# Kernel tuning notes

Hardware: AMD Instinct MI355X
Metric: run time of the kernel (lower is better)

Reference implementation:

```python
import jax, jax.numpy as jnp
import numpy as np

HEADS = 8
MODEL_DIM = 64
EPS = 1e-5


def _layernorm(x, gamma, beta):
    mu = jnp.mean(x, axis=-1, keepdims=True)
    var = jnp.var(x, axis=-1, keepdims=True)
    return (x - mu) * jax.lax.rsqrt(var + EPS) * gamma + beta


def setup_inputs() -> dict:
    key = jax.random.key(0)
    ks = jax.random.split(key, 5)
    bs, h, w, in_dim = 8, 32, 32, 512
    hd = HEADS * MODEL_DIM  # 512
    s = 0.02
    return {
        "x": jax.random.normal(ks[0], (bs, h, w, in_dim), jnp.float32),
        "Wq": jax.random.normal(ks[1], (in_dim, hd), jnp.float32) * s,
        "Wk": jax.random.normal(ks[2], (in_dim, hd), jnp.float32) * s,
        "Wv": jax.random.normal(ks[3], (in_dim, hd), jnp.float32) * s,
        "Wo": jax.random.normal(ks[4], (hd, in_dim), jnp.float32) * s,
        "gamma": jnp.ones((in_dim,), jnp.float32),
        "beta": jnp.zeros((in_dim,), jnp.float32),
    }


def reference(x, Wq, Wk, Wv, Wo, gamma, beta):
    bs, h, w, in_dim = x.shape
    # pre_norm=True: normalize first; residual uses the normalized x (as in original)
    xn = _layernorm(x, gamma, beta)
    Q = (xn @ Wq).reshape(bs, h, w, HEADS, MODEL_DIM)
    K = (xn @ Wk).reshape(bs, h, w, HEADS, MODEL_DIM)
    V = (xn @ Wv).reshape(bs, h, w, HEADS, MODEL_DIM)
    # full (h,w) x (h,w) correlation per head
    corr = jnp.einsum('bijhd,bklhd->bijhkl', Q, K) / jnp.sqrt(
        jnp.asarray(MODEL_DIM, x.dtype))
    cshape = corr.shape
    attn = jax.nn.softmax(corr.reshape(*cshape[:-2], -1), axis=-1).reshape(cshape)
    logits = jnp.einsum('bijhkl,bklhd->bijhd', attn, V).reshape(bs, h, w, -1)
    out = logits @ Wo + xn
    return out, attn
```

## Files before the change

### kernel.cpp

```cpp
#include <hip/hip_runtime.h>
#include <hip/hip_bf16.h>

typedef __attribute__((ext_vector_type(8))) short bf16x8;
typedef __attribute__((ext_vector_type(4))) short s16x4;
typedef __attribute__((ext_vector_type(4))) float f32x4;

#define DIM 512
#define NH 8
#define HD 64
#define SEQ 1024
#define NB 8
#define ROWS (NB*SEQ)

__device__ __forceinline__ short f2bf(float f) {
  union { float f; unsigned u; } v; v.f = f;
  unsigned r = v.u + 0x7fffu + ((v.u >> 16) & 1u);
  return (short)(r >> 16);
}
__device__ __forceinline__ float bf2f(short s) {
  union { unsigned u; float f; } v; v.u = ((unsigned)(unsigned short)s) << 16;
  return v.f;
}
__device__ __forceinline__ f32x4 mfma16(bf16x8 a, bf16x8 b, f32x4 c) {
  return __builtin_amdgcn_mfma_f32_16x16x32_bf16(a, b, c, 0, 0, 0);
}
__device__ __forceinline__ void gload16(const void* g, void* l) {
  __builtin_amdgcn_global_load_lds(
      (const __attribute__((address_space(1))) unsigned int*)g,
      (__attribute__((address_space(3))) unsigned int*)l, 16, 0, 0);
}
__device__ __forceinline__ void lds_barrier() {
  __builtin_amdgcn_sched_barrier(0);
  asm volatile("s_waitcnt lgkmcnt(0)" ::: "memory");
  __builtin_amdgcn_s_barrier();
  __builtin_amdgcn_sched_barrier(0);
}

__global__ __launch_bounds__(256) void prep_kernel(
    const float* __restrict__ x, const float* __restrict__ gamma,
    const float* __restrict__ beta, short* __restrict__ xnb,
    const float* __restrict__ Wq, const float* __restrict__ Wk,
    const float* __restrict__ Wv, const float* __restrict__ Wo,
    short* __restrict__ WqkvT, short* __restrict__ WoT) {
  __shared__ float tl[64 * 65];
  const int t = threadIdx.x;
  if (blockIdx.x < 2048) {
    const int row = blockIdx.x * 4 + (t >> 6);
    const int lane = t & 63;
    const float4* xr = reinterpret_cast<const float4*>(x + (size_t)row * DIM);
    const float4 a = xr[lane * 2], b2 = xr[lane * 2 + 1];
    float s = a.x + a.y + a.z + a.w + b2.x + b2.y + b2.z + b2.w;
    float sq = a.x*a.x + a.y*a.y + a.z*a.z + a.w*a.w +
               b2.x*b2.x + b2.y*b2.y + b2.z*b2.z + b2.w*b2.w;
    for (int off = 1; off < 64; off <<= 1) {
      s += __shfl_xor(s, off);
      sq += __shfl_xor(sq, off);
    }
    const float mean = s * (1.0f / DIM);
    const float var = sq * (1.0f / DIM) - mean * mean;
    const float rs = rsqrtf(var + 1e-5f);
    const float4 ga = reinterpret_cast<const float4*>(gamma)[lane * 2];
    const float4 gb = reinterpret_cast<const float4*>(gamma)[lane * 2 + 1];
    const float4 ba = reinterpret_cast<const float4*>(beta)[lane * 2];
    const float4 bb = reinterpret_cast<const float4*>(beta)[lane * 2 + 1];
    union { bf16x8 v; short sh[8]; } o;
    o.sh[0] = f2bf((a.x - mean) * rs * ga.x + ba.x);
    o.sh[1] = f2bf((a.y - mean) * rs * ga.y + ba.y);
    o.sh[2] = f2bf((a.z - mean) * rs * ga.z + ba.z);
    o.sh[3] = f2bf((a.w - mean) * rs * ga.w + ba.w);
    o.sh[4] = f2bf((b2.x - mean) * rs * gb.x + bb.x);
    o.sh[5] = f2bf((b2.y - mean) * rs * gb.y + bb.y);
    o.sh[6] = f2bf((b2.z - mean) * rs * gb.z + bb.z);
    o.sh[7] = f2bf((b2.w - mean) * rs * gb.w + bb.w);
    *reinterpret_cast<bf16x8*>(xnb + (size_t)row * DIM + lane * 8) = o.v;
  } else {
    const int bb = blockIdx.x - 2048;
    const int y = bb >> 6;
    const float* W = (y == 0) ? Wq : (y == 1) ? Wk : (y == 2) ? Wv : Wo;
    const int tile = bb & 63;
    const int k0 = (tile >> 3) * 64, n0 = (tile & 7) * 64;
#pragma unroll
    for (int i = 0; i < 16; ++i) {
      const int idx = i * 256 + t;
      const int k = idx >> 6, n = idx & 63;
      tl[n * 65 + k] = W[(size_t)(k0 + k) * 512 + n0 + n];
    }
    __syncthreads();
#pragma unroll
    for (int i = 0; i < 16; ++i) {
      const int idx = i * 256 + t;
      const int n = idx >> 6, k = idx & 63;
      const short v = f2bf(tl[n * 65 + k]);
      if (y < 3) WqkvT[(size_t)(y * 512 + n0 + n) * 512 + k0 + k] = v;
      else       WoT[(size_t)(n0 + n) * 512 + k0 + k] = v;
    }
  }
}

#define GEMM64_MAIN(A_, BT_, m0_, n0_)                                        \
  f32x4 acc[4][4] = {};                                                       \
  {                                                                           \
    const int srow = 8 * w + (lane >> 3);                                     \
    const int sseg = lane & 7;                                                \
    for (int kb = 0; kb < 512; kb += 64) {                                    \
      __syncthreads();                                                        \
      _Pragma("unroll")                                                       \
      for (int p = 0; p < 4; ++p) {                                           \
        const int r = 32 * p + srow;                                          \
        const int gs = 8 * (sseg ^ (r & 7));                                  \
        gload16(A_ + (size_t)(m0_ + r) * 512 + kb + gs,                       \
                &As[(32 * p + 8 * w) * 64]);                                  \
        gload16(BT_ + (size_t)(n0_ + r) * 512 + kb + gs,                      \
                &Bs[(32 * p + 8 * w) * 64]);                                  \
      }                                                                       \
      __syncthreads();                                                        \
      _Pragma("unroll")                                                       \
      for (int half = 0; half < 2; ++half) {                                  \
        bf16x8 af[4], bfr[4];                                                 \
        _Pragma("unroll")                                                     \
        for (int i = 0; i < 4; ++i) {                                         \
          const int ra = 64 * wr + 16 * i + c16;                              \
          af[i] = *reinterpret_cast<const bf16x8*>(                           \
              &As[ra * 64 + 8 * ((4 * half + g) ^ (ra & 7))]);                \
          const int rb = 64 * wc + 16 * i + c16;                              \
          bfr[i] = *reinterpret_cast<const bf16x8*>(                          \
              &Bs[rb * 64 + 8 * ((4 * half + g) ^ (rb & 7))]);                \
        }                                                                     \
        _Pragma("unroll")                                                     \
        for (int i = 0; i < 4; ++i)                                           \
          _Pragma("unroll")                                                   \
          for (int j = 0; j < 4; ++j)                                         \
            acc[i][j] = mfma16(af[i], bfr[j], acc[i][j]);                     \
      }                                                                       \
    }                                                                         \
  }

__global__ __launch_bounds__(256) void gemm_qkv(const short* __restrict__ A,
    const short* __restrict__ BT, short* __restrict__ Qo,
    short* __restrict__ Ko, short* __restrict__ VtF) {
  __shared__ short As[128 * 64];
  __shared__ short Bs[128 * 64];
  const int m0 = blockIdx.x * 128, n0 = blockIdx.y * 128;
  const int t = threadIdx.x, w = t >> 6, lane = t & 63, g = lane >> 4, c16 = lane & 15;
  const int wr = w >> 1, wc = w & 1;
  GEMM64_MAIN(A, BT, m0, n0)
  const int z = n0 >> 9;
  const int nl = n0 & 511;
  if (z < 2) {
    short* O = (z == 0) ? Qo : Ko;
#pragma unroll
    for (int i = 0; i < 4; ++i)
#pragma unroll
      for (int j = 0; j < 4; ++j) {
        const int row0 = m0 + 64 * wr + 16 * i + 4 * g;
        const int col = nl + 64 * wc + 16 * j + c16;
#pragma unroll
        for (int e = 0; e < 4; ++e)
          O[(size_t)(row0 + e) * 512 + col] = f2bf(acc[i][j][e]);
      }
  } else {
#pragma unroll
    for (int i = 0; i < 4; ++i)
#pragma unroll
      for (int j = 0; j < 4; ++j) {
        const int row0 = m0 + 64 * wr + 16 * i + 4 * g;
        const int col = nl + 64 * wc + 16 * j + c16;
        const int bb = row0 >> 10, ss0 = row0 & 1023, hh = col >> 6, dd = col & 63;
        const int cch = ss0 >> 7, kk = ss0 & 127;
        const int w2 = kk >> 5, g2 = (kk >> 3) & 3, ee0 = kk & 7;
        const int dt2 = dd >> 4, c162 = dd & 15;
        s16x4 pv;
#pragma unroll
        for (int e = 0; e < 4; ++e) pv[e] = f2bf(acc[i][j][e]);
        *reinterpret_cast<s16x4*>(
            &VtF[((size_t)((((bb * NH + hh) * 8 + cch) * 4 + w2) * 4 + dt2) << 9) +
                 (g2 * 16 + c162) * 8 + ee0]) = pv;
      }
  }
}

__global__ __launch_bounds__(256) void gemm_out(const short* __restrict__ A,
    const short* __restrict__ BT, const short* __restrict__ xnb,
    float* __restrict__ out) {
  __shared__ short As[128 * 64];
  __shared__ short Bs[128 * 64];
  const int m0 = blockIdx.x * 128, n0 = blockIdx.y * 128;
  const int t = threadIdx.x, w = t >> 6, lane = t & 63, g = lane >> 4, c16 = lane & 15;
  const int wr = w >> 1, wc = w & 1;
  GEMM64_MAIN(A, BT, m0, n0)
#pragma unroll
  for (int i = 0; i < 4; ++i)
#pragma unroll
    for (int j = 0; j < 4; ++j)
#pragma unroll
      for (int e = 0; e < 4; ++e) {
        const int row = m0 + 64 * wr + 16 * i + 4 * g + e;
        const int col = n0 + 64 * wc + 16 * j + c16;
        const size_t idx = (size_t)row * 512 + col;
        out[idx] = acc[i][j][e] + bf2f(xnb[idx]);
      }
}

__global__ __launch_bounds__(256, 2) void attn_kernel(
    const short* __restrict__ Qb, const short* __restrict__ Kb,
    const short* __restrict__ VtF, float* __restrict__ attnOut,
    short* __restrict__ Lg) {
  const int bid = blockIdx.x;
  const int rb = (bid >> 3) & 31;
  const int inst = (bid & 7) * 8 + (bid >> 8);
  const int b = inst >> 3, h = inst & 7;
  const int t = threadIdx.x;
  const int w = t >> 6, lane = t & 63, g = lane >> 4, c16 = lane & 15;
  const int rl = lane >> 3, sgl = lane & 7;

  __shared__ __align__(16) char smem[49664];
  __shared__ float red[2][4][16];
  short* Klds = (short*)smem;
  float* P32a = (float*)(smem + 32768);
  float* P32b = (float*)(smem + 41216);

  const short* qpa = Qb + ((size_t)(b * SEQ + rb * 32 + c16)) * DIM + h * HD + 8 * g;
  const bf16x8 qa0 = *reinterpret_cast<const bf16x8*>(qpa);
  const bf16x8 qa1 = *reinterpret_cast<const bf16x8*>(qpa + 32);
  const bf16x8 qB0 = *reinterpret_cast<const bf16x8*>(qpa + 16 * DIM);
  const bf16x8 qB1 = *reinterpret_cast<const bf16x8*>(qpa + 16 * DIM + 32);

  const short* kgbase = Kb + ((size_t)b * SEQ) * DIM + h * HD;
  const int swz = 8 * (sgl ^ rl);
  const int sw = c16 & 7;

#define KSTAGE(c_, buf_)                                                       \
  do {                                                                         \
    __builtin_amdgcn_sched_barrier(0);                                         \
    _Pragma("unroll") for (int i_ = 0; i_ < 4; ++i_) {                         \
      gload16(kgbase + (size_t)((c_) * 128 + 32 * w + 8 * i_ + rl) * DIM + swz,\
              &Klds[(buf_) * 8192 + (32 * w + 8 * i_) * 64]);                  \
    }                                                                          \
  } while (0)

  KSTAGE(0, 0);
  f32x4 acc[16] = {};
#pragma unroll
  for (int c = 0; c < 8; ++c) {
    if (c < 7) KSTAGE(c + 1, (c + 1) & 1);
    if (c < 7) { asm volatile("s_waitcnt vmcnt(4)" ::: "memory"); }
    else       { asm volatile("s_waitcnt vmcnt(0)" ::: "memory"); }
    __builtin_amdgcn_sched_barrier(0);
    const short* kl = &Klds[(c & 1) * 8192];
#pragma unroll
    for (int j = 0; j < 2; ++j) {
      const int lr = 32 * w + 16 * j + c16;
      bf16x8 k0 = *reinterpret_cast<const bf16x8*>(&kl[lr * 64 + 8 * (g ^ sw)]);
      bf16x8 k1 = *reinterpret_cast<const bf16x8*>(&kl[lr * 64 + 8 * ((g + 4) ^ sw)]);
      const int tt = c * 2 + j;
      acc[tt] = mfma16(k0, qa0, acc[tt]);
      acc[tt] = mfma16(k1, qa1, acc[tt]);
    }
  }

  const short* vf = VtF + (size_t)inst * 65536;
  bf16x8 vreg[4];
#pragma unroll
  for (int dt = 0; dt < 4; ++dt)
    vreg[dt] = *reinterpret_cast<const bf16x8*>(vf + (size_t)((w * 4 + dt) * 512) + lane * 8);
  bf16x8 kreg[4];
#pragma unroll
  for (int i = 0; i < 4; ++i)
    kreg[i] = *reinterpret_cast<const bf16x8*>(
        kgbase + (size_t)(32 * w + 8 * i + rl) * DIM + 8 * sgl);

  float m = -1e30f;
#pragma unroll
  for (int tt = 0; tt < 16; ++tt)
#pragma unroll
    for (int e = 0; e < 4; ++e) {
      acc[tt][e] *= 0.125f;
      m = fmaxf(m, acc[tt][e]);
    }
  m = fmaxf(m, __shfl_xor(m, 16));
  m = fmaxf(m, __shfl_xor(m, 32));
  if (g == 0) red[0][w][c16] = m;
  lds_barrier();
  m = fmaxf(fmaxf(red[0][0][c16], red[0][1][c16]),
            fmaxf(red[0][2][c16], red[0][3][c16]));
  float sm = 0.f;
#pragma unroll
  for (int tt = 0; tt < 16; ++tt)
#pragma unroll
    for (int e = 0; e < 4; ++e) {
      const float p = __expf(acc[tt][e] - m);
      acc[tt][e] = p;
      sm += p;
    }
  sm += __shfl_xor(sm, 16);
  sm += __shfl_xor(sm, 32);
  if (g == 0) red[1][w][c16] = sm;
  lds_barrier();
  const float rinvA = 1.0f / (red[1][0][c16] + red[1][1][c16] +
                              red[1][2][c16] + red[1][3][c16]);

  bf16x8 pA[8];
#pragma unroll
  for (int c = 0; c < 8; ++c) {
    union { bf16x8 v; short sh[8]; } u;
#pragma unroll
    for (int j = 0; j < 2; ++j)
#pragma unroll
      for (int e = 0; e < 4; ++e)
        u.sh[4 * j + e] = f2bf(acc[2 * c + j][e] * rinvA);
    pA[c] = u.v;
  }
#pragma unroll
  for (int tt = 0; tt < 16; ++tt)
#pragma unroll
    for (int e = 0; e < 4; ++e) acc[tt][e] = 0.f;

  f32x4 paccA[4] = {};
  const int qrow = t >> 4, qs = t & 15;
  float* astore = attnOut + (size_t)b * 8388608 +
                  (size_t)(rb * 32 + qrow) * 8192 + h * 1024;
#pragma unroll
  for (int c = 0; c < 8; ++c) {
    lds_barrier();
#pragma unroll
    for (int i = 0; i < 4; ++i)
      *reinterpret_cast<bf16x8*>(
          &Klds[(c & 1) * 8192 + (32 * w + 8 * i + rl) * 64 + 8 * (sgl ^ rl)]) = kreg[i];
    {
      float* P32w = (c & 1) ? P32b : P32a;
      union { bf16x8 v; short sh[8]; } u; u.v = pA[c];
      f32x4 v0, v1;
#pragma unroll
      for (int e = 0; e < 4; ++e) { v0[e] = bf2f(u.sh[e]); v1[e] = bf2f(u.sh[4 + e]); }
      *reinterpret_cast<f32x4*>(&P32w[c16 * 132 + 32 * w + 4 * g]) = v0;
      *reinterpret_cast<f32x4*>(&P32w[c16 * 132 + 32 * w + 16 + 4 * g]) = v1;
    }
    if (c < 7) {
#pragma unroll
      for (int i = 0; i < 4; ++i)
        kreg[i] = *reinterpret_cast<const bf16x8*>(
            kgbase + (size_t)((c + 1) * 128 + 32 * w + 8 * i + rl) * DIM + 8 * sgl);
    }
    lds_barrier();
    {
      const float* P32r = (c & 1) ? P32b : P32a;
      const f32x4 s0 = *reinterpret_cast<const f32x4*>(&P32r[qrow * 132 + 4 * qs]);
      const f32x4 s1 = *reinterpret_cast<const f32x4*>(&P32r[qrow * 132 + 64 + 4 * qs]);
      __builtin_nontemporal_store(s0, reinterpret_cast<f32x4*>(astore + c * 128 + 4 * qs));
      __builtin_nontemporal_store(s1, reinterpret_cast<f32x4*>(astore + c * 128 + 64 + 4 * qs));
    }
    const short* kl = &Klds[(c & 1) * 8192];
#pragma unroll
    for (int j = 0; j < 2; ++j) {
      const int lr = 32 * w + 16 * j + c16;
      bf16x8 k0 = *reinterpret_cast<const bf16x8*>(&kl[lr * 64 + 8 * (g ^ sw)]);
      bf16x8 k1 = *reinterpret_cast<const bf16x8*>(&kl[lr * 64 + 8 * ((g + 4) ^ sw)]);
      const int tt = c * 2 + j;
      acc[tt] = mfma16(k0, qB0, acc[tt]);
      acc[tt] = mfma16(k1, qB1, acc[tt]);
    }
#pragma unroll
    for (int dt = 0; dt < 4; ++dt)
      paccA[dt] = mfma16(pA[c], vreg[dt], paccA[dt]);
    if (c < 7) {
#pragma unroll
      for (int dt = 0; dt < 4; ++dt)
        vreg[dt] = *reinterpret_cast<const bf16x8*>(
            vf + (size_t)((((c + 1) * 4 + w) * 4 + dt) * 512) + lane * 8);
    }
  }

#pragma unroll
  for (int dt = 0; dt < 4; ++dt)
    vreg[dt] = *reinterpret_cast<const bf16x8*>(vf + (size_t)((w * 4 + dt) * 512) + lane * 8);

  float mB = -1e30f;
#pragma unroll
  for (int tt = 0; tt < 16; ++tt)
#pragma unroll
    for (int e = 0; e < 4; ++e) {
      acc[tt][e] *= 0.125f;
      mB = fmaxf(mB, acc[tt][e]);
    }
  mB = fmaxf(mB, __shfl_xor(mB, 16));
  mB = fmaxf(mB, __shfl_xor(mB, 32));
  if (g == 0) red[0][w][c16] = mB;
  lds_barrier();
  mB = fmaxf(fmaxf(red[0][0][c16], red[0][1][c16]),
             fmaxf(red[0][2][c16], red[0][3][c16]));
  float smB = 0.f;
#pragma unroll
  for (int tt = 0; tt < 16; ++tt)
#pragma unroll
    for (int e = 0; e < 4; ++e) {
      const float p = __expf(acc[tt][e] - mB);
      acc[tt][e] = p;
      smB += p;
    }
  smB += __shfl_xor(smB, 16);
  smB += __shfl_xor(smB, 32);
  if (g == 0) red[1][w][c16] = smB;
  lds_barrier();
  const float rinvB = 1.0f / (red[1][0][c16] + red[1][1][c16] +
                              red[1][2][c16] + red[1][3][c16]);
  bf16x8 pB[8];
#pragma unroll
  for (int c = 0; c < 8; ++c) {
    union { bf16x8 v; short sh[8]; } u;
#pragma unroll
    for (int j = 0; j < 2; ++j)
#pragma unroll
      for (int e = 0; e < 4; ++e)
        u.sh[4 * j + e] = f2bf(acc[2 * c + j][e] * rinvB);
    pB[c] = u.v;
  }

  f32x4 paccB[4] = {};
  float* astoreB = astore + 16 * 8192;
#pragma unroll
  for (int c = 0; c < 8; ++c) {
    lds_barrier();
    {
      float* P32w = (c & 1) ? P32b : P32a;
      union { bf16x8 v; short sh[8]; } u; u.v = pB[c];
      f32x4 v0, v1;
#pragma unroll
      for (int e = 0; e < 4; ++e) { v0[e] = bf2f(u.sh[e]); v1[e] = bf2f(u.sh[4 + e]); }
      *reinterpret_cast<f32x4*>(&P32w[c16 * 132 + 32 * w + 4 * g]) = v0;
      *reinterpret_cast<f32x4*>(&P32w[c16 * 132 + 32 * w + 16 + 4 * g]) = v1;
    }
    lds_barrier();
    {
      const float* P32r = (c & 1) ? P32b : P32a;
      const f32x4 s0 = *reinterpret_cast<const f32x4*>(&P32r[qrow * 132 + 4 * qs]);
      const f32x4 s1 = *reinterpret_cast<const f32x4*>(&P32r[qrow * 132 + 64 + 4 * qs]);
      __builtin_nontemporal_store(s0, reinterpret_cast<f32x4*>(astoreB + c * 128 + 4 * qs));
      __builtin_nontemporal_store(s1, reinterpret_cast<f32x4*>(astoreB + c * 128 + 64 + 4 * qs));
    }
#pragma unroll
    for (int dt = 0; dt < 4; ++dt)
      paccB[dt] = mfma16(pB[c], vreg[dt], paccB[dt]);
    if (c < 7) {
#pragma unroll
      for (int dt = 0; dt < 4; ++dt)
        vreg[dt] = *reinterpret_cast<const bf16x8*>(
            vf + (size_t)((((c + 1) * 4 + w) * 4 + dt) * 512) + lane * 8);
    }
  }

  lds_barrier();
  f32x4* red2 = reinterpret_cast<f32x4*>(smem);
#pragma unroll
  for (int dt = 0; dt < 4; ++dt) red2[(w * 4 + dt) * 64 + lane] = paccA[dt];
  lds_barrier();
  {
    const int dt = w;
    f32x4 s = red2[dt * 64 + lane];
#pragma unroll
    for (int w2 = 1; w2 < 4; ++w2) {
      f32x4 o = red2[(w2 * 4 + dt) * 64 + lane];
#pragma unroll
      for (int e = 0; e < 4; ++e) s[e] += o[e];
    }
    short* lrow = Lg + ((size_t)(b * SEQ + rb * 32 + 4 * g)) * DIM + h * HD + 16 * dt + c16;
#pragma unroll
    for (int e = 0; e < 4; ++e) lrow[(size_t)e * DIM] = f2bf(s[e]);
  }
  lds_barrier();
#pragma unroll
  for (int dt = 0; dt < 4; ++dt) red2[(w * 4 + dt) * 64 + lane] = paccB[dt];
  lds_barrier();
  {
    const int dt = w;
    f32x4 s = red2[dt * 64 + lane];
#pragma unroll
    for (int w2 = 1; w2 < 4; ++w2) {
      f32x4 o = red2[(w2 * 4 + dt) * 64 + lane];
#pragma unroll
      for (int e = 0; e < 4; ++e) s[e] += o[e];
    }
    short* lrow = Lg + ((size_t)(b * SEQ + rb * 32 + 16 + 4 * g)) * DIM + h * HD + 16 * dt + c16;
#pragma unroll
    for (int e = 0; e < 4; ++e) lrow[(size_t)e * DIM] = f2bf(s[e]);
  }
}

extern "C" void kernel_launch(void* const* d_in, const int* in_sizes, int n_in,
                              void* d_out, int out_size, void* d_ws, size_t ws_size,
                              hipStream_t stream) {
  const float* x = (const float*)d_in[0];
  const float* Wq = (const float*)d_in[1];
  const float* Wk = (const float*)d_in[2];
  const float* Wv = (const float*)d_in[3];
  const float* Wo = (const float*)d_in[4];
  const float* gamma = (const float*)d_in[5];
  const float* beta = (const float*)d_in[6];
  float* out = (float*)d_out;
  float* attn = out + (size_t)ROWS * DIM;

  char* ws = (char*)d_ws;
  short* xnb = (short*)ws;
  short* WqkvT = (short*)(ws + (size_t)8 * 1024 * 1024);
  short* WoT = WqkvT + 1536 * 512;
  short* Qb = (short*)(ws + (size_t)10 * 1024 * 1024);
  short* Kbp = (short*)(ws + (size_t)18 * 1024 * 1024);
  short* VtF = (short*)(ws + (size_t)26 * 1024 * 1024);
  short* Lg = (short*)(ws + (size_t)34 * 1024 * 1024);

  prep_kernel<<<2304, 256, 0, stream>>>(x, gamma, beta, xnb, Wq, Wk, Wv, Wo, WqkvT, WoT);
  gemm_qkv<<<dim3(64, 12), 256, 0, stream>>>(xnb, WqkvT, Qb, Kbp, VtF);
  attn_kernel<<<2048, 256, 0, stream>>>(Qb, Kbp, VtF, attn, Lg);
  gemm_out<<<dim3(64, 4), 256, 0, stream>>>(Lg, WoT, xnb, out);
}
```

Measured before the change: 122.0 us.

## Halve attention-loop barriers by deferring P stores and prefetching K two chunks ahead

In both softmax-probability loops, the global store of each attention chunk is moved to the next iteration, after the single remaining barrier, with an epilogue store for the last chunk. This removes one LDS barrier per iteration. K tiles are now written to LDS one iteration early and loaded from global memory two chunks ahead, so the K load has more time to complete. The V-transpose output indexing in the projection GEMM is also remapped so the key order in each 8-element group matches the packing of the P fragments used by the PV MFMA, which looks like a correctness fix.

```diff
diff --git a/kernel.cpp b/kernel.cpp
--- a/kernel.cpp
+++ b/kernel.cpp
@@ -167,7 +167,9 @@
         const int col = nl + 64 * wc + 16 * j + c16;
         const int bb = row0 >> 10, ss0 = row0 & 1023, hh = col >> 6, dd = col & 63;
         const int cch = ss0 >> 7, kk = ss0 & 127;
-        const int w2 = kk >> 5, g2 = (kk >> 3) & 3, ee0 = kk & 7;
+        const int w2 = kk >> 5;
+        const int g2 = (kk >> 2) & 3;
+        const int ee0 = 4 * ((kk >> 4) & 1) + (kk & 3);
         const int dt2 = dd >> 4, c162 = dd & 15;
         s16x4 pv;
 #pragma unroll
@@ -320,12 +322,23 @@
   float* astore = attnOut + (size_t)b * 8388608 +
                   (size_t)(rb * 32 + qrow) * 8192 + h * 1024;
 #pragma unroll
+  for (int i = 0; i < 4; ++i)
+    *reinterpret_cast<bf16x8*>(
+        &Klds[(32 * w + 8 * i + rl) * 64 + 8 * (sgl ^ rl)]) = kreg[i];
+#pragma unroll
+  for (int i = 0; i < 4; ++i)
+    kreg[i] = *reinterpret_cast<const bf16x8*>(
+        kgbase + (size_t)(128 + 32 * w + 8 * i + rl) * DIM + 8 * sgl);
+#pragma unroll
   for (int c = 0; c < 8; ++c) {
     lds_barrier();
-#pragma unroll
-    for (int i = 0; i < 4; ++i)
-      *reinterpret_cast<bf16x8*>(
-          &Klds[(c & 1) * 8192 + (32 * w + 8 * i + rl) * 64 + 8 * (sgl ^ rl)]) = kreg[i];
+    if (c >= 1) {
+      const float* P32r = ((c - 1) & 1) ? P32b : P32a;
+      const f32x4 s0 = *reinterpret_cast<const f32x4*>(&P32r[qrow * 132 + 4 * qs]);
+      const f32x4 s1 = *reinterpret_cast<const f32x4*>(&P32r[qrow * 132 + 64 + 4 * qs]);
+      __builtin_nontemporal_store(s0, reinterpret_cast<f32x4*>(astore + (c - 1) * 128 + 4 * qs));
+      __builtin_nontemporal_store(s1, reinterpret_cast<f32x4*>(astore + (c - 1) * 128 + 64 + 4 * qs));
+    }
     {
       float* P32w = (c & 1) ? P32b : P32a;
       union { bf16x8 v; short sh[8]; } u; u.v = pA[c];
@@ -338,16 +351,8 @@
     if (c < 7) {
 #pragma unroll
       for (int i = 0; i < 4; ++i)
-        kreg[i] = *reinterpret_cast<const bf16x8*>(
-            kgbase + (size_t)((c + 1) * 128 + 32 * w + 8 * i + rl) * DIM + 8 * sgl);
-    }
-    lds_barrier();
-    {
-      const float* P32r = (c & 1) ? P32b : P32a;
-      const f32x4 s0 = *reinterpret_cast<const f32x4*>(&P32r[qrow * 132 + 4 * qs]);
-      const f32x4 s1 = *reinterpret_cast<const f32x4*>(&P32r[qrow * 132 + 64 + 4 * qs]);
-      __builtin_nontemporal_store(s0, reinterpret_cast<f32x4*>(astore + c * 128 + 4 * qs));
-      __builtin_nontemporal_store(s1, reinterpret_cast<f32x4*>(astore + c * 128 + 64 + 4 * qs));
+        *reinterpret_cast<bf16x8*>(
+            &Klds[((c + 1) & 1) * 8192 + (32 * w + 8 * i + rl) * 64 + 8 * (sgl ^ rl)]) = kreg[i];
     }
     const short* kl = &Klds[(c & 1) * 8192];
 #pragma unroll
@@ -362,12 +367,25 @@
 #pragma unroll
     for (int dt = 0; dt < 4; ++dt)
       paccA[dt] = mfma16(pA[c], vreg[dt], paccA[dt]);
+    if (c < 6) {
+#pragma unroll
+      for (int i = 0; i < 4; ++i)
+        kreg[i] = *reinterpret_cast<const bf16x8*>(
+            kgbase + (size_t)((c + 2) * 128 + 32 * w + 8 * i + rl) * DIM + 8 * sgl);
+    }
     if (c < 7) {
 #pragma unroll
       for (int dt = 0; dt < 4; ++dt)
         vreg[dt] = *reinterpret_cast<const bf16x8*>(
             vf + (size_t)((((c + 1) * 4 + w) * 4 + dt) * 512) + lane * 8);
     }
+  }
+  lds_barrier();
+  {
+    const f32x4 s0 = *reinterpret_cast<const f32x4*>(&P32b[qrow * 132 + 4 * qs]);
+    const f32x4 s1 = *reinterpret_cast<const f32x4*>(&P32b[qrow * 132 + 64 + 4 * qs]);
+    __builtin_nontemporal_store(s0, reinterpret_cast<f32x4*>(astore + 7 * 128 + 4 * qs));
+    __builtin_nontemporal_store(s1, reinterpret_cast<f32x4*>(astore + 7 * 128 + 64 + 4 * qs));
   }
 
 #pragma unroll
@@ -420,6 +438,13 @@
 #pragma unroll
   for (int c = 0; c < 8; ++c) {
     lds_barrier();
+    if (c >= 1) {
+      const float* P32r = ((c - 1) & 1) ? P32b : P32a;
+      const f32x4 s0 = *reinterpret_cast<const f32x4*>(&P32r[qrow * 132 + 4 * qs]);
+      const f32x4 s1 = *reinterpret_cast<const f32x4*>(&P32r[qrow * 132 + 64 + 4 * qs]);
+      __builtin_nontemporal_store(s0, reinterpret_cast<f32x4*>(astoreB + (c - 1) * 128 + 4 * qs));
+      __builtin_nontemporal_store(s1, reinterpret_cast<f32x4*>(astoreB + (c - 1) * 128 + 64 + 4 * qs));
+    }
     {
       float* P32w = (c & 1) ? P32b : P32a;
       union { bf16x8 v; short sh[8]; } u; u.v = pB[c];
@@ -429,14 +454,6 @@
       *reinterpret_cast<f32x4*>(&P32w[c16 * 132 + 32 * w + 4 * g]) = v0;
       *reinterpret_cast<f32x4*>(&P32w[c16 * 132 + 32 * w + 16 + 4 * g]) = v1;
     }
-    lds_barrier();
-    {
-      const float* P32r = (c & 1) ? P32b : P32a;
-      const f32x4 s0 = *reinterpret_cast<const f32x4*>(&P32r[qrow * 132 + 4 * qs]);
-      const f32x4 s1 = *reinterpret_cast<const f32x4*>(&P32r[qrow * 132 + 64 + 4 * qs]);
-      __builtin_nontemporal_store(s0, reinterpret_cast<f32x4*>(astoreB + c * 128 + 4 * qs));
-      __builtin_nontemporal_store(s1, reinterpret_cast<f32x4*>(astoreB + c * 128 + 64 + 4 * qs));
-    }
 #pragma unroll
     for (int dt = 0; dt < 4; ++dt)
       paccB[dt] = mfma16(pB[c], vreg[dt], paccB[dt]);
@@ -446,6 +463,13 @@
         vreg[dt] = *reinterpret_cast<const bf16x8*>(
             vf + (size_t)((((c + 1) * 4 + w) * 4 + dt) * 512) + lane * 8);
     }
+  }
+  lds_barrier();
+  {
+    const f32x4 s0 = *reinterpret_cast<const f32x4*>(&P32b[qrow * 132 + 4 * qs]);
+    const f32x4 s1 = *reinterpret_cast<const f32x4*>(&P32b[qrow * 132 + 64 + 4 * qs]);
+    __builtin_nontemporal_store(s0, reinterpret_cast<f32x4*>(astoreB + 7 * 128 + 4 * qs));
+    __builtin_nontemporal_store(s1, reinterpret_cast<f32x4*>(astoreB + 7 * 128 + 64 + 4 * qs));
   }
 
   lds_barrier();
```

After: 126.1 us. +3.4%, slower.

## Shrink attention LDS footprint with single swizzled P staging buffer and reused reductions

Applied to the files above, without the earlier changes.

The attention kernel's LDS allocation shrinks by replacing the two padded fp32 P staging buffers with one XOR-swizzled buffer and placing the softmax reduction scratch inside it. An extra barrier protects the reused region. The V-fragment permutation written by the projection GEMM also changes its k-index mapping, which must match how the P fragments pair with V in the MFMA. The aim is lower LDS use so more workgroups fit per CU, and the swizzle is meant to avoid bank conflicts without padding. The cost is losing the double buffer for P, which may serialize store phases.

```diff
diff --git a/kernel.cpp b/kernel.cpp
--- a/kernel.cpp
+++ b/kernel.cpp
@@ -167,7 +167,9 @@
         const int col = nl + 64 * wc + 16 * j + c16;
         const int bb = row0 >> 10, ss0 = row0 & 1023, hh = col >> 6, dd = col & 63;
         const int cch = ss0 >> 7, kk = ss0 & 127;
-        const int w2 = kk >> 5, g2 = (kk >> 3) & 3, ee0 = kk & 7;
+        const int w2 = kk >> 5;
+        const int g2 = (kk >> 2) & 3;
+        const int ee0 = 4 * ((kk >> 4) & 1) + (kk & 3);
         const int dt2 = dd >> 4, c162 = dd & 15;
         s16x4 pv;
 #pragma unroll
@@ -213,11 +215,11 @@
   const int w = t >> 6, lane = t & 63, g = lane >> 4, c16 = lane & 15;
   const int rl = lane >> 3, sgl = lane & 7;
 
-  __shared__ __align__(16) char smem[49664];
-  __shared__ float red[2][4][16];
+  __shared__ __align__(16) char smem[40960];
   short* Klds = (short*)smem;
-  float* P32a = (float*)(smem + 32768);
-  float* P32b = (float*)(smem + 41216);
+  float* P32 = (float*)(smem + 32768);
+  float* redm = P32;
+  float* reds = P32 + 64;
 
   const short* qpa = Qb + ((size_t)(b * SEQ + rb * 32 + c16)) * DIM + h * HD + 8 * g;
   const bf16x8 qa0 = *reinterpret_cast<const bf16x8*>(qpa);
@@ -228,6 +230,7 @@
   const short* kgbase = Kb + ((size_t)b * SEQ) * DIM + h * HD;
   const int swz = 8 * (sgl ^ rl);
   const int sw = c16 & 7;
+  const int sw32 = 4 * (c16 & 7);
 
 #define KSTAGE(c_, buf_)                                                       \
   do {                                                                         \
@@ -279,10 +282,10 @@
     }
   m = fmaxf(m, __shfl_xor(m, 16));
   m = fmaxf(m, __shfl_xor(m, 32));
-  if (g == 0) red[0][w][c16] = m;
-  lds_barrier();
-  m = fmaxf(fmaxf(red[0][0][c16], red[0][1][c16]),
-            fmaxf(red[0][2][c16], red[0][3][c16]));
+  if (g == 0) redm[w * 16 + c16] = m;
+  lds_barrier();
+  m = fmaxf(fmaxf(redm[c16], redm[16 + c16]),
+            fmaxf(redm[32 + c16], redm[48 + c16]));
   float sm = 0.f;
 #pragma unroll
   for (int tt = 0; tt < 16; ++tt)
@@ -294,10 +297,10 @@
     }
   sm += __shfl_xor(sm, 16);
   sm += __shfl_xor(sm, 32);
-  if (g == 0) red[1][w][c16] = sm;
-  lds_barrier();
-  const float rinvA = 1.0f / (red[1][0][c16] + red[1][1][c16] +
-                              red[1][2][c16] + red[1][3][c16]);
+  if (g == 0) reds[w * 16 + c16] = sm;
+  lds_barrier();
+  const float rinvA = 1.0f / (reds[c16] + reds[16 + c16] +
+                              reds[32 + c16] + reds[48 + c16]);
 
   bf16x8 pA[8];
 #pragma unroll
@@ -317,6 +320,7 @@
 
   f32x4 paccA[4] = {};
   const int qrow = t >> 4, qs = t & 15;
+  const int rsw = 4 * (qrow & 7);
   float* astore = attnOut + (size_t)b * 8388608 +
                   (size_t)(rb * 32 + qrow) * 8192 + h * 1024;
 #pragma unroll
@@ -327,13 +331,12 @@
       *reinterpret_cast<bf16x8*>(
           &Klds[(c & 1) * 8192 + (32 * w + 8 * i + rl) * 64 + 8 * (sgl ^ rl)]) = kreg[i];
     {
-      float* P32w = (c & 1) ? P32b : P32a;
       union { bf16x8 v; short sh[8]; } u; u.v = pA[c];
       f32x4 v0, v1;
 #pragma unroll
       for (int e = 0; e < 4; ++e) { v0[e] = bf2f(u.sh[e]); v1[e] = bf2f(u.sh[4 + e]); }
-      *reinterpret_cast<f32x4*>(&P32w[c16 * 132 + 32 * w + 4 * g]) = v0;
-      *reinterpret_cast<f32x4*>(&P32w[c16 * 132 + 32 * w + 16 + 4 * g]) = v1;
+      *reinterpret_cast<f32x4*>(&P32[c16 * 128 + ((32 * w + 4 * g) ^ sw32)]) = v0;
+      *reinterpret_cast<f32x4*>(&P32[c16 * 128 + ((32 * w + 16 + 4 * g) ^ sw32)]) = v1;
     }
     if (c < 7) {
 #pragma unroll
@@ -343,9 +346,8 @@
     }
     lds_barrier();
     {
-      const float* P32r = (c & 1) ? P32b : P32a;
-      const f32x4 s0 = *reinterpret_cast<const f32x4*>(&P32r[qrow * 132 + 4 * qs]);
-      const f32x4 s1 = *reinterpret_cast<const f32x4*>(&P32r[qrow * 132 + 64 + 4 * qs]);
+      const f32x4 s0 = *reinterpret_cast<const f32x4*>(&P32[qrow * 128 + ((4 * qs) ^ rsw)]);
+      const f32x4 s1 = *reinterpret_cast<const f32x4*>(&P32[qrow * 128 + ((64 + 4 * qs) ^ rsw)]);
       __builtin_nontemporal_store(s0, reinterpret_cast<f32x4*>(astore + c * 128 + 4 * qs));
       __builtin_nontemporal_store(s1, reinterpret_cast<f32x4*>(astore + c * 128 + 64 + 4 * qs));
     }
@@ -384,10 +386,11 @@
     }
   mB = fmaxf(mB, __shfl_xor(mB, 16));
   mB = fmaxf(mB, __shfl_xor(mB, 32));
-  if (g == 0) red[0][w][c16] = mB;
-  lds_barrier();
-  mB = fmaxf(fmaxf(red[0][0][c16], red[0][1][c16]),
-             fmaxf(red[0][2][c16], red[0][3][c16]));
+  lds_barrier();
+  if (g == 0) redm[w * 16 + c16] = mB;
+  lds_barrier();
+  mB = fmaxf(fmaxf(redm[c16], redm[16 + c16]),
+             fmaxf(redm[32 + c16], redm[48 + c16]));
   float smB = 0.f;
 #pragma unroll
   for (int tt = 0; tt < 16; ++tt)
@@ -399,10 +402,10 @@
     }
   smB += __shfl_xor(smB, 16);
   smB += __shfl_xor(smB, 32);
-  if (g == 0) red[1][w][c16] = smB;
-  lds_barrier();
-  const float rinvB = 1.0f / (red[1][0][c16] + red[1][1][c16] +
-                              red[1][2][c16] + red[1][3][c16]);
+  if (g == 0) reds[w * 16 + c16] = smB;
+  lds_barrier();
+  const float rinvB = 1.0f / (reds[c16] + reds[16 + c16] +
+                              reds[32 + c16] + reds[48 + c16]);
   bf16x8 pB[8];
 #pragma unroll
   for (int c = 0; c < 8; ++c) {
@@ -421,19 +424,17 @@
   for (int c = 0; c < 8; ++c) {
     lds_barrier();
     {
-      float* P32w = (c & 1) ? P32b : P32a;
       union { bf16x8 v; short sh[8]; } u; u.v = pB[c];
       f32x4 v0, v1;
 #pragma unroll
       for (int e = 0; e < 4; ++e) { v0[e] = bf2f(u.sh[e]); v1[e] = bf2f(u.sh[4 + e]); }
-      *reinterpret_cast<f32x4*>(&P32w[c16 * 132 + 32 * w + 4 * g]) = v0;
-      *reinterpret_cast<f32x4*>(&P32w[c16 * 132 + 32 * w + 16 + 4 * g]) = v1;
+      *reinterpret_cast<f32x4*>(&P32[c16 * 128 + ((32 * w + 4 * g) ^ sw32)]) = v0;
+      *reinterpret_cast<f32x4*>(&P32[c16 * 128 + ((32 * w + 16 + 4 * g) ^ sw32)]) = v1;
     }
     lds_barrier();
     {
-      const float* P32r = (c & 1) ? P32b : P32a;
-      const f32x4 s0 = *reinterpret_cast<const f32x4*>(&P32r[qrow * 132 + 4 * qs]);
-      const f32x4 s1 = *reinterpret_cast<const f32x4*>(&P32r[qrow * 132 + 64 + 4 * qs]);
+      const f32x4 s0 = *reinterpret_cast<const f32x4*>(&P32[qrow * 128 + ((4 * qs) ^ rsw)]);
+      const f32x4 s1 = *reinterpret_cast<const f32x4*>(&P32[qrow * 128 + ((64 + 4 * qs) ^ rsw)]);
       __builtin_nontemporal_store(s0, reinterpret_cast<f32x4*>(astoreB + c * 128 + 4 * qs));
       __builtin_nontemporal_store(s1, reinterpret_cast<f32x4*>(astoreB + c * 128 + 64 + 4 * qs));
     }
```

After: 119.8 us, median of 2. No clear change (-1.8%).
